# Performance work log

Hardware: AMD Instinct MI355X
Metric: run time of the kernel (lower is better)

The kernel has to match this reference:

```python
import jax, jax.numpy as jnp
import numpy as np

NUM_CLASSES = 10
NPTS = 100            # quadrature points per unit interval (torch default npts=100)
EPS = 1e-5            # self.epsilon in the torch module
BATCH = 131072
C_IN = 512


def _betaln(a, b):
    return jax.lax.lgamma(a) + jax.lax.lgamma(b) - jax.lax.lgamma(a + b)


def setup_inputs() -> dict:
    key = jax.random.key(0)
    k1, k2, k3, k4, k5 = jax.random.split(key, 5)
    s = 1.0 / np.sqrt(C_IN).astype(np.float32)
    x = jax.random.normal(k1, (BATCH, C_IN), dtype=jnp.float32)
    W_alpha = jax.random.normal(k2, (C_IN, 1), dtype=jnp.float32) * s
    b_alpha = jax.random.normal(k3, (1,), dtype=jnp.float32) * s
    W_beta = jax.random.normal(k4, (C_IN, 1), dtype=jnp.float32) * s
    b_beta = jax.random.normal(k5, (1,), dtype=jnp.float32) * s
    return {"x": x, "W_alpha": W_alpha, "b_alpha": b_alpha,
            "W_beta": W_beta, "b_beta": b_beta}


def reference(x, W_alpha, b_alpha, W_beta, b_beta):
    # alpha, beta: [B, 1], clamp(1 + softplus(linear(x)), 1, 100)
    alpha = jnp.clip(1.0 + jax.nn.softplus(x @ W_alpha + b_alpha), 1.0, 100.0)
    beta = jnp.clip(1.0 + jax.nn.softplus(x @ W_beta + b_beta), 1.0, 100.0)
    lbeta = _betaln(alpha, beta)  # [B, 1] log Beta-function normalizer
    dx = 1.0 / (NPTS * NUM_CLASSES)

    def unnorm_cdf(b_thr):
        # torch: linspace(eps, b-eps, int(npts*b)); Beta.log_prob broadcast [B, n]
        n = int(NPTS * b_thr)
        if n == 0:
            return jnp.zeros((x.shape[0],), dtype=x.dtype)
        grid = jnp.linspace(EPS, b_thr - EPS, n, dtype=x.dtype)  # [n]
        logpdf = ((alpha - 1.0) * jnp.log(grid)
                  + (beta - 1.0) * jnp.log1p(-grid)
                  - lbeta)  # [B, n]
        return jnp.exp(logpdf).sum(axis=1) * dx  # [B]

    # thresholds i/C for i = 0..C (static Python loop over C+1 small fixed set)
    cdfs = [unnorm_cdf(i / NUM_CLASSES) for i in range(NUM_CLASSES + 1)]
    probs = jnp.stack([cdfs[i + 1] - cdfs[i] for i in range(NUM_CLASSES)], axis=1)  # [B, C]
    # torch uses diag(1/rowsum) @ probs == row-broadcast normalization
    return probs / probs.sum(axis=1, keepdims=True)
```

## Files before the change

kernel.cpp:

```cpp
#include <hip/hip_runtime.h>
#include <math.h>

#define EPS_F 1e-5f
#define NPOINTS 550
#define CIN 512

static __device__ __forceinline__ float softplus_f(float z) {
    return fmaxf(z, 0.0f) + log1pf(expf(-fabsf(z)));
}

static __device__ __forceinline__ float dot8(const float4 a0, const float4 a1,
                                             const float4 w0, const float4 w1) {
    float s = a0.x * w0.x;
    s = fmaf(a0.y, w0.y, s);
    s = fmaf(a0.z, w0.z, s);
    s = fmaf(a0.w, w0.w, s);
    s = fmaf(a1.x, w1.x, s);
    s = fmaf(a1.y, w1.y, s);
    s = fmaf(a1.z, w1.z, s);
    s = fmaf(a1.w, w1.w, s);
    return s;
}

__global__ __launch_bounds__(256, 4) void beta_unimodal_kernel(
    const float* __restrict__ x,
    const float* __restrict__ Wa, const float* __restrict__ ba,
    const float* __restrict__ Wb, const float* __restrict__ bb,
    float* __restrict__ out)
{
    __shared__ float2 tab[NPOINTS];

    const int tid = threadIdx.x;

    for (int p = tid; p < NPOINTS; p += 256) {
        int i = 1, off = 0;
        while (p >= off + 10 * i) { off += 10 * i; ++i; }
        const int j = p - off;
        const int n = 10 * i;
        const float thr = (float)i * 0.1f;
        const float step = (thr - 2.0f * EPS_F) / (float)(n - 1);
        const float g = EPS_F + step * (float)j;
        float2 e;
        e.x = log2f(g);
        e.y = log2f(1.0f - g);
        tab[p] = e;
    }
    __syncthreads();

    const int lane = tid & 63;
    const int wave = tid >> 6;
    const long rowBase = ((long)blockIdx.x * 4 + wave) * 64;

    const float4* Wa4 = (const float4*)Wa;
    const float4* Wb4 = (const float4*)Wb;
    const float4 wa0 = Wa4[lane], wa1 = Wa4[64 + lane];
    const float4 wb0 = Wb4[lane], wb1 = Wb4[64 + lane];

    float my_da = 0.0f, my_db = 0.0f;

    for (int r0 = 0; r0 < 64; r0 += 4) {
        float4 xs0[4], xs1[4];
        #pragma unroll
        for (int u = 0; u < 4; ++u) {
            const float4* xr = (const float4*)(x + (rowBase + r0 + u) * CIN);
            xs0[u] = xr[lane];
            xs1[u] = xr[64 + lane];
        }
        #pragma unroll
        for (int u = 0; u < 4; ++u) {
            float da = dot8(xs0[u], xs1[u], wa0, wa1);
            float db = dot8(xs0[u], xs1[u], wb0, wb1);
            #pragma unroll
            for (int s = 32; s > 0; s >>= 1) {
                da += __shfl_xor(da, s, 64);
                db += __shfl_xor(db, s, 64);
            }
            if (lane == r0 + u) { my_da = da; my_db = db; }
        }
    }

    const float za = my_da + ba[0];
    const float zb = my_db + bb[0];
    const float alpha = fminf(fmaxf(1.0f + softplus_f(za), 1.0f), 100.0f);
    const float beta  = fminf(fmaxf(1.0f + softplus_f(zb), 1.0f), 100.0f);
    const float am1 = alpha - 1.0f;
    const float bm1 = beta - 1.0f;

    const float denom = am1 + bm1;
    float mode = (denom > 0.0f) ? (am1 / denom) : 0.5f;
    mode = fminf(fmaxf(mode, 1e-7f), 1.0f - 1.1920929e-7f);
    const float M2 = am1 * log2f(mode) + bm1 * log2f(1.0f - mode);

    float cum[11];
    cum[0] = 0.0f;
    int p = 0;
    #pragma unroll
    for (int i = 1; i <= 10; ++i) {
        const int n = 10 * i;
        float s0 = 0.0f, s1 = 0.0f;
        for (int j = 0; j < n; j += 2) {
            const float2 t0 = tab[p];
            const float2 t1 = tab[p + 1];
            p += 2;
            const float e0 = fmaf(am1, t0.x, bm1 * t0.y) - M2;
            const float e1 = fmaf(am1, t1.x, bm1 * t1.y) - M2;
            s0 += __builtin_amdgcn_exp2f(e0);
            s1 += __builtin_amdgcn_exp2f(e1);
        }
        cum[i] = s0 + s1;
    }

    const float inv = 1.0f / cum[10];
    float* orow = out + (rowBase + lane) * 10;
    #pragma unroll
    for (int k = 0; k < 10; ++k) orow[k] = (cum[k + 1] - cum[k]) * inv;
}

extern "C" void kernel_launch(void* const* d_in, const int* in_sizes, int n_in,
                              void* d_out, int out_size, void* d_ws, size_t ws_size,
                              hipStream_t stream) {
    const float* x  = (const float*)d_in[0];
    const float* Wa = (const float*)d_in[1];
    const float* ba = (const float*)d_in[2];
    const float* Wb = (const float*)d_in[3];
    const float* bb = (const float*)d_in[4];
    float* out = (float*)d_out;

    const int batch = in_sizes[0] / CIN;
    const int blocks = batch / 256;
    beta_unimodal_kernel<<<blocks, 256, 0, stream>>>(x, Wa, ba, Wb, bb, out);
}
```

Measured before the change: 421.1 us.

## Split each row's quadrature across four lanes and stage output through LDS

Each block now handles 64 rows instead of 256, and each row's quadrature is spread across four lanes. Each lane sums every fourth point, and the partials are combined with xor shuffles. The dot-product phase now covers 16 rows per wave instead of 64. Output is staged in shared memory and written back with coalesced float4 stores. This cuts the serial exp2 work per lane and raises the block count and occupancy target. In exchange, each block rebuilds the log table for fewer rows, and there is an extra barrier and more shuffles.

```diff
diff --git a/kernel.cpp b/kernel.cpp
--- a/kernel.cpp
+++ b/kernel.cpp
@@ -22,13 +22,14 @@
     return s;
 }
 
-__global__ __launch_bounds__(256, 4) void beta_unimodal_kernel(
+__global__ __launch_bounds__(256, 8) void beta_unimodal_kernel(
     const float* __restrict__ x,
     const float* __restrict__ Wa, const float* __restrict__ ba,
     const float* __restrict__ Wb, const float* __restrict__ bb,
     float* __restrict__ out)
 {
     __shared__ float2 tab[NPOINTS];
+    __shared__ float outbuf[64 * 10];
 
     const int tid = threadIdx.x;
 
@@ -49,16 +50,18 @@
 
     const int lane = tid & 63;
     const int wave = tid >> 6;
-    const long rowBase = ((long)blockIdx.x * 4 + wave) * 64;
+    const long rowBase = (long)blockIdx.x * 64 + wave * 16;
 
     const float4* Wa4 = (const float4*)Wa;
     const float4* Wb4 = (const float4*)Wb;
     const float4 wa0 = Wa4[lane], wa1 = Wa4[64 + lane];
     const float4 wb0 = Wb4[lane], wb1 = Wb4[64 + lane];
 
+    const int g = lane >> 2;
+    const int q = lane & 3;
     float my_da = 0.0f, my_db = 0.0f;
 
-    for (int r0 = 0; r0 < 64; r0 += 4) {
+    for (int r0 = 0; r0 < 16; r0 += 4) {
         float4 xs0[4], xs1[4];
         #pragma unroll
         for (int u = 0; u < 4; ++u) {
@@ -75,7 +78,7 @@
                 da += __shfl_xor(da, s, 64);
                 db += __shfl_xor(db, s, 64);
             }
-            if (lane == r0 + u) { my_da = da; my_db = db; }
+            if (g == r0 + u) { my_da = da; my_db = db; }
         }
     }
 
@@ -91,29 +94,36 @@
     mode = fminf(fmaxf(mode, 1e-7f), 1.0f - 1.1920929e-7f);
     const float M2 = am1 * log2f(mode) + bm1 * log2f(1.0f - mode);
 
-    float cum[11];
-    cum[0] = 0.0f;
-    int p = 0;
+    float seg[10];
+    int p0 = 0;
     #pragma unroll
     for (int i = 1; i <= 10; ++i) {
         const int n = 10 * i;
-        float s0 = 0.0f, s1 = 0.0f;
-        for (int j = 0; j < n; j += 2) {
-            const float2 t0 = tab[p];
-            const float2 t1 = tab[p + 1];
-            p += 2;
-            const float e0 = fmaf(am1, t0.x, bm1 * t0.y) - M2;
-            const float e1 = fmaf(am1, t1.x, bm1 * t1.y) - M2;
-            s0 += __builtin_amdgcn_exp2f(e0);
-            s1 += __builtin_amdgcn_exp2f(e1);
+        float s = 0.0f;
+        for (int j = q; j < n; j += 4) {
+            const float2 t = tab[p0 + j];
+            const float e = fmaf(am1, t.x, bm1 * t.y) - M2;
+            s += __builtin_amdgcn_exp2f(e);
         }
-        cum[i] = s0 + s1;
+        s += __shfl_xor(s, 1, 64);
+        s += __shfl_xor(s, 2, 64);
+        seg[i - 1] = s;
+        p0 += n;
     }
 
-    const float inv = 1.0f / cum[10];
-    float* orow = out + (rowBase + lane) * 10;
-    #pragma unroll
-    for (int k = 0; k < 10; ++k) orow[k] = (cum[k + 1] - cum[k]) * inv;
+    const float inv = 1.0f / seg[9];
+    const int rowLocal = wave * 16 + g;
+    for (int k = q; k < 10; k += 4) {
+        const float prev = (k > 0) ? seg[k - 1] : 0.0f;
+        outbuf[rowLocal * 10 + k] = (seg[k] - prev) * inv;
+    }
+    __syncthreads();
+
+    if (tid < 160) {
+        const float4* src = (const float4*)outbuf;
+        float4* dst = (float4*)(out + (size_t)blockIdx.x * 640);
+        dst[tid] = src[tid];
+    }
 }
 
 extern "C" void kernel_launch(void* const* d_in, const int* in_sizes, int n_in,
@@ -127,6 +137,6 @@
     float* out = (float*)d_out;
 
     const int batch = in_sizes[0] / CIN;
-    const int blocks = batch / 256;
+    const int blocks = batch / 64;
     beta_unimodal_kernel<<<blocks, 256, 0, stream>>>(x, Wa, ba, Wb, bb, out);
 }
```

Measured after the change: 367.4 us. 12.8% less time.
